# Kernel optimization log

Hardware: AMD Instinct MI355X
Metric: run time of the kernel (lower is better)

## Reference

```python
import jax, jax.numpy as jnp
import numpy as np

N_NODES = 100000


def mean_aggregate(x, src, dst, n_nodes):
    # gather messages from src nodes, mean-reduce onto dst nodes (DGL copy_u + mean)
    msg = x[src]                                                  # [E, d]
    summed = jax.ops.segment_sum(msg, dst, num_segments=n_nodes)  # [N, d]
    cnt = jax.ops.segment_sum(jnp.ones((src.shape[0],), x.dtype), dst,
                              num_segments=n_nodes)               # [N]
    # zero in-degree nodes get mean 0 (matches DGL mean reducer)
    return summed / jnp.maximum(cnt, 1.0)[:, None]


def setup_inputs() -> dict:
    key = jax.random.key(0)
    ks = jax.random.split(key, 7)
    E = 1600000
    d_in, d_hid, d_out = 128, 128, 128
    features = jax.random.normal(ks[0], (N_NODES, d_in), dtype=jnp.float32)
    src = jax.random.randint(ks[1], (E,), 0, N_NODES, dtype=jnp.int64)
    dst = jax.random.randint(ks[2], (E,), 0, N_NODES, dtype=jnp.int64)
    W1 = jax.random.normal(ks[3], (d_hid, d_in), dtype=jnp.float32) * (1.0 / np.sqrt(d_in))
    b1 = jax.random.normal(ks[4], (d_hid,), dtype=jnp.float32) * 0.01
    W2 = jax.random.normal(ks[5], (d_out, d_hid), dtype=jnp.float32) * (1.0 / np.sqrt(d_hid))
    b2 = jax.random.normal(ks[6], (d_out,), dtype=jnp.float32) * 0.01
    return {"features": features, "src": src, "dst": dst,
            "W1": W1, "b1": b1, "W2": W2, "b2": b2}


def reference(features, src, dst, W1, b1, W2, b2):
    # GINConv (eps=0, mean agg): h = Linear((1+eps)*x + mean_neigh(x))
    agg1 = mean_aggregate(features, src, dst, N_NODES)
    x1 = jax.nn.relu(jnp.dot(features + agg1, W1.T) + b1)   # layer1 + outer relu
    agg2 = mean_aggregate(x1, src, dst, N_NODES)
    x2 = jnp.dot(x1 + agg2, W2.T) + b2                       # layer2, no activation
    return x2
```

## Files before the change

### kernel.cpp

```cpp
#include <hip/hip_runtime.h>

#define D 128
#define BIN_SHIFT 7
#define BIN_NODES 128
#define FRAG_CAP 32
#define NBLK_A 256
#define CAP_B 2560

typedef __attribute__((ext_vector_type(8))) short bf16x8;
typedef __attribute__((ext_vector_type(4))) float f32x4;

static __device__ __forceinline__ unsigned short f2bf(float f) {
    unsigned int u = __float_as_uint(f);
    unsigned int r = (u + 0x7fffu + ((u >> 16) & 1u)) >> 16;
    return (unsigned short)r;
}
static __device__ __forceinline__ float bf2f(unsigned short u) {
    return __uint_as_float((unsigned int)u << 16);
}

__global__ void f2bf_kernel(const float4* __restrict__ in, ushort4* __restrict__ out, int n4) {
    int i = blockIdx.x * blockDim.x + threadIdx.x;
    if (i >= n4) return;
    float4 v = in[i];
    out[i] = make_ushort4(f2bf(v.x), f2bf(v.y), f2bf(v.z), f2bf(v.w));
}
__global__ void wconv2_kernel(const float* __restrict__ W1, const float* __restrict__ W2,
                              unsigned short* __restrict__ Wb1, unsigned short* __restrict__ Wb2,
                              int n) {
    int i = blockIdx.x * blockDim.x + threadIdx.x;
    if (i < n)            Wb1[i] = f2bf(W1[i]);
    else if (i < 2 * n)   Wb2[i - n] = f2bf(W2[i - n]);
}

__global__ __launch_bounds__(1024) void binA_kernel(const int* __restrict__ src,
                                                    const int* __restrict__ dst, int E,
                                                    int NB, int* __restrict__ gcnt,
                                                    unsigned int* __restrict__ ebufA) {
    __shared__ int cnt[1024];
    int t = threadIdx.x;
    cnt[t] = 0;
    __syncthreads();
    int per = (E + gridDim.x - 1) / gridDim.x;
    int start = blockIdx.x * per;
    int endb = min(start + per, E);
    int f = blockIdx.x;
    for (int i = start + t; i < endb; i += blockDim.x) {
        int s = src[i], d = dst[i];
        int b = d >> BIN_SHIFT;
        unsigned int val = ((unsigned int)(d & (BIN_NODES - 1)) << 17) | (unsigned int)s;
        int p = atomicAdd(&cnt[b], 1);
        if (p < FRAG_CAP)
            ebufA[((size_t)b * NBLK_A + f) * FRAG_CAP + p] = val;
    }
    __syncthreads();
    if (t < NB) gcnt[(size_t)t * NBLK_A + f] = min(cnt[t], FRAG_CAP);
}

__global__ __launch_bounds__(256) void binB_kernel(const unsigned int* __restrict__ ebufA,
                                                   const int* __restrict__ gcnt,
                                                   int NB, int N,
                                                   int* __restrict__ src_sorted,
                                                   int* __restrict__ row_beg,
                                                   int* __restrict__ deg_g) {
    __shared__ int gc[NBLK_A];
    __shared__ int h[BIN_NODES];
    __shared__ int h2[BIN_NODES];
    __shared__ int part[BIN_NODES];
    int b = blockIdx.x, t = threadIdx.x;
    gc[t] = gcnt[(size_t)b * NBLK_A + t];
    if (t < BIN_NODES) h[t] = 0;
    __syncthreads();

    const uint4* base = (const uint4*)(ebufA + (size_t)b * NBLK_A * FRAG_CAP);
    uint4 vals[8];
    unsigned int vmask[8];
#pragma unroll
    for (int k = 0; k < 8; ++k) {
        int c = t + k * 256;
        vals[k] = base[c];
        int frag = c >> 3;
        int sb = (c & 7) * 4;
        int cc = gc[frag];
        int nv = cc - sb;
        nv = max(0, min(4, nv));
        vmask[k] = nv;
    }
#pragma unroll
    for (int k = 0; k < 8; ++k) {
        unsigned int nv = vmask[k];
        if (nv > 0) atomicAdd(&h[(vals[k].x >> 17) & (BIN_NODES - 1)], 1);
        if (nv > 1) atomicAdd(&h[(vals[k].y >> 17) & (BIN_NODES - 1)], 1);
        if (nv > 2) atomicAdd(&h[(vals[k].z >> 17) & (BIN_NODES - 1)], 1);
        if (nv > 3) atomicAdd(&h[(vals[k].w >> 17) & (BIN_NODES - 1)], 1);
    }
    __syncthreads();
    if (t < BIN_NODES) part[t] = h[t];
    __syncthreads();
    for (int off = 1; off < BIN_NODES; off <<= 1) {
        int x = 0;
        if (t < BIN_NODES && t >= off) x = part[t - off];
        __syncthreads();
        if (t < BIN_NODES) part[t] += x;
        __syncthreads();
    }
    if (t < BIN_NODES) {
        int excl = part[t] - h[t];
        int node = (b << BIN_SHIFT) + t;
        if (node < N) { row_beg[node] = b * CAP_B + excl; deg_g[node] = h[t]; }
        h2[t] = excl;
    }
    __syncthreads();
    int* seg = src_sorted + (size_t)b * CAP_B;
#pragma unroll
    for (int k = 0; k < 8; ++k) {
        unsigned int nv = vmask[k];
        if (nv > 0) seg[atomicAdd(&h2[(vals[k].x >> 17) & (BIN_NODES - 1)], 1)] = (int)(vals[k].x & 0x1FFFFu);
        if (nv > 1) seg[atomicAdd(&h2[(vals[k].y >> 17) & (BIN_NODES - 1)], 1)] = (int)(vals[k].y & 0x1FFFFu);
        if (nv > 2) seg[atomicAdd(&h2[(vals[k].z >> 17) & (BIN_NODES - 1)], 1)] = (int)(vals[k].z & 0x1FFFFu);
        if (nv > 3) seg[atomicAdd(&h2[(vals[k].w >> 17) & (BIN_NODES - 1)], 1)] = (int)(vals[k].w & 0x1FFFFu);
    }
}

#define ACC8(v)                                           \
    do {                                                  \
        a0 += __uint_as_float((v).x << 16);               \
        a1 += __uint_as_float((v).x & 0xffff0000u);       \
        a2 += __uint_as_float((v).y << 16);               \
        a3 += __uint_as_float((v).y & 0xffff0000u);       \
        a4 += __uint_as_float((v).z << 16);               \
        a5 += __uint_as_float((v).z & 0xffff0000u);       \
        a6 += __uint_as_float((v).w << 16);               \
        a7 += __uint_as_float((v).w & 0xffff0000u);       \
    } while (0)

__global__ __launch_bounds__(256) void aggregate_bf16(const uint4* __restrict__ x,
                                                      const int* __restrict__ row_beg,
                                                      const int* __restrict__ deg_g,
                                                      const int* __restrict__ src_sorted,
                                                      uint4* __restrict__ out, int N) {
    int node = blockIdx.x * 16 + (threadIdx.x >> 4);
    if (node >= N) return;
    int c = threadIdx.x & 15;
    int beg = row_beg[node];
    int dg  = deg_g[node];
    int end = beg + dg;
    float a0 = 0.f, a1 = 0.f, a2 = 0.f, a3 = 0.f, a4 = 0.f, a5 = 0.f, a6 = 0.f, a7 = 0.f;
    int j = beg;
    for (; j + 8 <= end; j += 8) {
        int s0 = src_sorted[j + 0], s1 = src_sorted[j + 1];
        int s2 = src_sorted[j + 2], s3 = src_sorted[j + 3];
        int s4 = src_sorted[j + 4], s5 = src_sorted[j + 5];
        int s6 = src_sorted[j + 6], s7 = src_sorted[j + 7];
        uint4 v0 = x[(size_t)s0 * 16 + c];
        uint4 v1 = x[(size_t)s1 * 16 + c];
        uint4 v2 = x[(size_t)s2 * 16 + c];
        uint4 v3 = x[(size_t)s3 * 16 + c];
        uint4 v4 = x[(size_t)s4 * 16 + c];
        uint4 v5 = x[(size_t)s5 * 16 + c];
        uint4 v6 = x[(size_t)s6 * 16 + c];
        uint4 v7 = x[(size_t)s7 * 16 + c];
        ACC8(v0); ACC8(v1); ACC8(v2); ACC8(v3);
        ACC8(v4); ACC8(v5); ACC8(v6); ACC8(v7);
    }
    for (; j + 4 <= end; j += 4) {
        int s0 = src_sorted[j + 0], s1 = src_sorted[j + 1];
        int s2 = src_sorted[j + 2], s3 = src_sorted[j + 3];
        uint4 v0 = x[(size_t)s0 * 16 + c];
        uint4 v1 = x[(size_t)s1 * 16 + c];
        uint4 v2 = x[(size_t)s2 * 16 + c];
        uint4 v3 = x[(size_t)s3 * 16 + c];
        ACC8(v0); ACC8(v1); ACC8(v2); ACC8(v3);
    }
    for (; j < end; ++j) {
        int s = src_sorted[j];
        uint4 v = x[(size_t)s * 16 + c];
        ACC8(v);
    }
    float inv = 1.0f / fmaxf((float)dg, 1.0f);
    uint4 xv = x[(size_t)node * 16 + c];
    float f0 = __uint_as_float(xv.x << 16)          + a0 * inv;
    float f1 = __uint_as_float(xv.x & 0xffff0000u)  + a1 * inv;
    float f2 = __uint_as_float(xv.y << 16)          + a2 * inv;
    float f3 = __uint_as_float(xv.y & 0xffff0000u)  + a3 * inv;
    float f4 = __uint_as_float(xv.z << 16)          + a4 * inv;
    float f5 = __uint_as_float(xv.z & 0xffff0000u)  + a5 * inv;
    float f6 = __uint_as_float(xv.w << 16)          + a6 * inv;
    float f7 = __uint_as_float(xv.w & 0xffff0000u)  + a7 * inv;
    uint4 r;
    r.x = (unsigned int)f2bf(f0) | ((unsigned int)f2bf(f1) << 16);
    r.y = (unsigned int)f2bf(f2) | ((unsigned int)f2bf(f3) << 16);
    r.z = (unsigned int)f2bf(f4) | ((unsigned int)f2bf(f5) << 16);
    r.w = (unsigned int)f2bf(f6) | ((unsigned int)f2bf(f7) << 16);
    out[(size_t)node * 16 + c] = r;
}

__global__ __launch_bounds__(256) void gemm_mfma(const unsigned short* __restrict__ A,
                                                 const unsigned short* __restrict__ Wb,
                                                 const float* __restrict__ bias,
                                                 unsigned short* __restrict__ outb,
                                                 float* __restrict__ outf,
                                                 int N, int relu) {
    int t = threadIdx.x;
    int wave = t >> 6;
    int lane = t & 63;
    int quad = lane >> 4;
    int l16  = lane & 15;
    int row0 = blockIdx.x * 128 + wave * 32;

    f32x4 acc[2][8];
#pragma unroll
    for (int rt = 0; rt < 2; ++rt)
#pragma unroll
        for (int ct = 0; ct < 8; ++ct)
            acc[rt][ct] = (f32x4){0.f, 0.f, 0.f, 0.f};

    const unsigned short* a0 = A + (size_t)(row0 + l16) * D + quad * 8;
    const unsigned short* a1 = a0 + (size_t)16 * D;
    bool ok0 = (row0 + l16) < N;
    bool ok1 = (row0 + 16 + l16) < N;
    bf16x8 zz = {0, 0, 0, 0, 0, 0, 0, 0};

#pragma unroll
    for (int ks = 0; ks < 4; ++ks) {
        bf16x8 af0 = ok0 ? *(const bf16x8*)(a0 + ks * 32) : zz;
        bf16x8 af1 = ok1 ? *(const bf16x8*)(a1 + ks * 32) : zz;
#pragma unroll
        for (int ct = 0; ct < 8; ++ct) {
            bf16x8 bfr = *(const bf16x8*)(Wb + (size_t)(ct * 16 + l16) * D + ks * 32 + quad * 8);
            acc[0][ct] = __builtin_amdgcn_mfma_f32_16x16x32_bf16(af0, bfr, acc[0][ct], 0, 0, 0);
            acc[1][ct] = __builtin_amdgcn_mfma_f32_16x16x32_bf16(af1, bfr, acc[1][ct], 0, 0, 0);
        }
    }

#pragma unroll
    for (int rt = 0; rt < 2; ++rt) {
        int rbase = row0 + rt * 16 + quad * 4;
#pragma unroll
        for (int ct = 0; ct < 8; ++ct) {
            int col = ct * 16 + l16;
            float bb = bias[col];
#pragma unroll
            for (int r = 0; r < 4; ++r) {
                int row = rbase + r;
                if (row < N) {
                    float v = acc[rt][ct][r] + bb;
                    if (relu) v = fmaxf(v, 0.f);
                    if (outb) outb[(size_t)row * D + col] = f2bf(v);
                    else      outf[(size_t)row * D + col] = v;
                }
            }
        }
    }
}

extern "C" void kernel_launch(void* const* d_in, const int* in_sizes, int n_in,
                              void* d_out, int out_size, void* d_ws, size_t ws_size,
                              hipStream_t stream) {
    const float* features = (const float*)d_in[0];
    const int*   src      = (const int*)d_in[1];
    const int*   dst      = (const int*)d_in[2];
    const float* W1       = (const float*)d_in[3];
    const float* b1       = (const float*)d_in[4];
    const float* W2       = (const float*)d_in[5];
    const float* b2       = (const float*)d_in[6];
    float* out = (float*)d_out;

    int N = in_sizes[0] / D;
    int E = in_sizes[1];
    int NB = (N + BIN_NODES - 1) >> BIN_SHIFT;

    char* ws = (char*)d_ws;
    size_t off = 0;
    unsigned short* bufA = (unsigned short*)(ws + off); off += (size_t)N * D * 2;
    unsigned short* bufB = (unsigned short*)(ws + off); off += (size_t)N * D * 2;
    unsigned short* Wb1  = (unsigned short*)(ws + off); off += (size_t)D * D * 2;
    unsigned short* Wb2  = (unsigned short*)(ws + off); off += (size_t)D * D * 2;
    int* gcnt    = (int*)(ws + off); off += (size_t)NB * NBLK_A * 4;
    int* row_beg = (int*)(ws + off); off += (size_t)N * 4;
    int* deg_g   = (int*)(ws + off); off += (size_t)N * 4;

    unsigned int* ebufA = (unsigned int*)d_out;
    int* src_sorted = (int*)((char*)d_out + (size_t)NB * NBLK_A * FRAG_CAP * 4);

    f2bf_kernel<<<(N * 32 + 255) / 256, 256, 0, stream>>>(
        (const float4*)features, (ushort4*)bufA, N * 32);
    wconv2_kernel<<<(2 * D * D + 255) / 256, 256, 0, stream>>>(W1, W2, Wb1, Wb2, D * D);

    binA_kernel<<<NBLK_A, 1024, 0, stream>>>(src, dst, E, NB, gcnt, ebufA);
    binB_kernel<<<NB, 256, 0, stream>>>(ebufA, gcnt, NB, N, src_sorted, row_beg, deg_g);

    int gemm_grid = (N + 127) / 128;

    aggregate_bf16<<<(N + 15) / 16, 256, 0, stream>>>(
        (const uint4*)bufA, row_beg, deg_g, src_sorted, (uint4*)bufB, N);
    gemm_mfma<<<gemm_grid, 256, 0, stream>>>(bufB, Wb1, b1, bufA, (float*)nullptr, N, 1);

    aggregate_bf16<<<(N + 15) / 16, 256, 0, stream>>>(
        (const uint4*)bufA, row_beg, deg_g, src_sorted, (uint4*)bufB, N);
    gemm_mfma<<<gemm_grid, 256, 0, stream>>>(bufB, Wb2, b2, (unsigned short*)nullptr, out, N, 0);
}
```

Baseline: 350.1 us.

## Fuse neighbor mean aggregation with MFMA GEMM into one kernel per layer

Adds an agg_gemm kernel in which each block gathers and mean-reduces 128 node rows straight into swizzled LDS, then runs the bf16 MFMA linear layer with bias and optional ReLU from that tile. This removes the intermediate aggregated buffer's global write and re-read and one launch per layer. To allow fusing layer 2 (whose output goes to d_out), src_sorted moves into the workspace when it fits, with the old two-kernel path kept as a fallback. The cost is 32KB of LDS per block, which lowers occupancy for the latency-bound gather phase.

New measurement: 385.0 us. 1.1x slower.

```diff
diff --git a/kernel.cpp b/kernel.cpp
--- a/kernel.cpp
+++ b/kernel.cpp
@@ -134,16 +134,9 @@
         a7 += __uint_as_float((v).w & 0xffff0000u);       \
     } while (0)
 
-__global__ __launch_bounds__(256) void aggregate_bf16(const uint4* __restrict__ x,
-                                                      const int* __restrict__ row_beg,
-                                                      const int* __restrict__ deg_g,
-                                                      const int* __restrict__ src_sorted,
-                                                      uint4* __restrict__ out, int N) {
-    int node = blockIdx.x * 16 + (threadIdx.x >> 4);
-    if (node >= N) return;
-    int c = threadIdx.x & 15;
-    int beg = row_beg[node];
-    int dg  = deg_g[node];
+static __device__ __forceinline__ uint4 gather_mean_row(const uint4* __restrict__ x,
+                                                        const int* __restrict__ src_sorted,
+                                                        int beg, int dg, int c, int node) {
     int end = beg + dg;
     float a0 = 0.f, a1 = 0.f, a2 = 0.f, a3 = 0.f, a4 = 0.f, a5 = 0.f, a6 = 0.f, a7 = 0.f;
     int j = beg;
@@ -192,7 +185,98 @@
     r.y = (unsigned int)f2bf(f2) | ((unsigned int)f2bf(f3) << 16);
     r.z = (unsigned int)f2bf(f4) | ((unsigned int)f2bf(f5) << 16);
     r.w = (unsigned int)f2bf(f6) | ((unsigned int)f2bf(f7) << 16);
-    out[(size_t)node * 16 + c] = r;
+    return r;
+}
+
+__global__ __launch_bounds__(256) void agg_gemm(const uint4* __restrict__ x,
+                                                const int* __restrict__ row_beg,
+                                                const int* __restrict__ deg_g,
+                                                const int* __restrict__ src_sorted,
+                                                const unsigned short* __restrict__ Wb,
+                                                const float* __restrict__ bias,
+                                                unsigned short* __restrict__ outb,
+                                                float* __restrict__ outf,
+                                                int N, int relu) {
+    __shared__ unsigned short sA[128 * 128];
+    int t = threadIdx.x;
+    int b = blockIdx.x;
+    int g = t >> 4;
+    int c = t & 15;
+
+    for (int rep = 0; rep < 8; ++rep) {
+        int nl = rep * 16 + g;
+        int node = b * 128 + nl;
+        uint4 r = {0u, 0u, 0u, 0u};
+        if (node < N) {
+            int beg = row_beg[node];
+            int dg  = deg_g[node];
+            r = gather_mean_row(x, src_sorted, beg, dg, c, node);
+        }
+        int slot = c ^ (nl & 7);
+        *(uint4*)&sA[nl * 128 + slot * 8] = r;
+    }
+    __syncthreads();
+
+    int wave = t >> 6;
+    int lane = t & 63;
+    int quad = lane >> 4;
+    int l16  = lane & 15;
+    int row0 = b * 128 + wave * 32;
+    int rl0 = wave * 32 + l16;
+    int rl1 = rl0 + 16;
+
+    f32x4 acc[2][8];
+#pragma unroll
+    for (int rt = 0; rt < 2; ++rt)
+#pragma unroll
+        for (int ct = 0; ct < 8; ++ct)
+            acc[rt][ct] = (f32x4){0.f, 0.f, 0.f, 0.f};
+
+#pragma unroll
+    for (int ks = 0; ks < 4; ++ks) {
+        int s = ks * 4 + quad;
+        bf16x8 af0 = *(const bf16x8*)&sA[rl0 * 128 + (s ^ (rl0 & 7)) * 8];
+        bf16x8 af1 = *(const bf16x8*)&sA[rl1 * 128 + (s ^ (rl1 & 7)) * 8];
+#pragma unroll
+        for (int ct = 0; ct < 8; ++ct) {
+            bf16x8 bfr = *(const bf16x8*)(Wb + (size_t)(ct * 16 + l16) * D + ks * 32 + quad * 8);
+            acc[0][ct] = __builtin_amdgcn_mfma_f32_16x16x32_bf16(af0, bfr, acc[0][ct], 0, 0, 0);
+            acc[1][ct] = __builtin_amdgcn_mfma_f32_16x16x32_bf16(af1, bfr, acc[1][ct], 0, 0, 0);
+        }
+    }
+
+#pragma unroll
+    for (int rt = 0; rt < 2; ++rt) {
+        int rbase = row0 + rt * 16 + quad * 4;
+#pragma unroll
+        for (int ct = 0; ct < 8; ++ct) {
+            int col = ct * 16 + l16;
+            float bb = bias[col];
+#pragma unroll
+            for (int r = 0; r < 4; ++r) {
+                int row = rbase + r;
+                if (row < N) {
+                    float v = acc[rt][ct][r] + bb;
+                    if (relu) v = fmaxf(v, 0.f);
+                    if (outb) outb[(size_t)row * D + col] = f2bf(v);
+                    else      outf[(size_t)row * D + col] = v;
+                }
+            }
+        }
+    }
+}
+
+__global__ __launch_bounds__(256) void aggregate_bf16(const uint4* __restrict__ x,
+                                                      const int* __restrict__ row_beg,
+                                                      const int* __restrict__ deg_g,
+                                                      const int* __restrict__ src_sorted,
+                                                      uint4* __restrict__ out, int N) {
+    int node = blockIdx.x * 16 + (threadIdx.x >> 4);
+    if (node >= N) return;
+    int c = threadIdx.x & 15;
+    int beg = row_beg[node];
+    int dg  = deg_g[node];
+    out[(size_t)node * 16 + c] = gather_mean_row(x, src_sorted, beg, dg, c, node);
 }
 
 __global__ __launch_bounds__(256) void gemm_mfma(const unsigned short* __restrict__ A,
@@ -281,7 +365,10 @@
     int* deg_g   = (int*)(ws + off); off += (size_t)N * 4;
 
     unsigned int* ebufA = (unsigned int*)d_out;
-    int* src_sorted = (int*)((char*)d_out + (size_t)NB * NBLK_A * FRAG_CAP * 4);
+    size_t ss_bytes = (size_t)NB * CAP_B * 4;
+    bool ss_in_ws = (ws_size >= off + ss_bytes);
+    int* src_sorted = ss_in_ws ? (int*)(ws + off)
+                               : (int*)((char*)d_out + (size_t)NB * NBLK_A * FRAG_CAP * 4);
 
     f2bf_kernel<<<(N * 32 + 255) / 256, 256, 0, stream>>>(
         (const float4*)features, (ushort4*)bufA, N * 32);
@@ -290,13 +377,18 @@
     binA_kernel<<<NBLK_A, 1024, 0, stream>>>(src, dst, E, NB, gcnt, ebufA);
     binB_kernel<<<NB, 256, 0, stream>>>(ebufA, gcnt, NB, N, src_sorted, row_beg, deg_g);
 
-    int gemm_grid = (N + 127) / 128;
-
-    aggregate_bf16<<<(N + 15) / 16, 256, 0, stream>>>(
-        (const uint4*)bufA, row_beg, deg_g, src_sorted, (uint4*)bufB, N);
-    gemm_mfma<<<gemm_grid, 256, 0, stream>>>(bufB, Wb1, b1, bufA, (float*)nullptr, N, 1);
-
-    aggregate_bf16<<<(N + 15) / 16, 256, 0, stream>>>(
-        (const uint4*)bufA, row_beg, deg_g, src_sorted, (uint4*)bufB, N);
-    gemm_mfma<<<gemm_grid, 256, 0, stream>>>(bufB, Wb2, b2, (unsigned short*)nullptr, out, N, 0);
-}
+    agg_gemm<<<NB, 256, 0, stream>>>(
+        (const uint4*)bufA, row_beg, deg_g, src_sorted, Wb1, b1,
+        bufB, (float*)nullptr, N, 1);
+
+    if (ss_in_ws) {
+        agg_gemm<<<NB, 256, 0, stream>>>(
+            (const uint4*)bufB, row_beg, deg_g, src_sorted, Wb2, b2,
+            (unsigned short*)nullptr, out, N, 0);
+    } else {
+        aggregate_bf16<<<(N + 15) / 16, 256, 0, stream>>>(
+            (const uint4*)bufB, row_beg, deg_g, src_sorted, (uint4*)bufA, N);
+        gemm_mfma<<<(N + 127) / 128, 256, 0, stream>>>(
+            bufA, Wb2, b2, (unsigned short*)nullptr, out, N, 0);
+    }
+}
```
